# Kernel tuning notes

Measured on AMD Instinct MI355X. Metric: run time of the kernel, lower is better.

## Reference

```python
import jax, jax.numpy as jnp
import numpy as np
import itertools

SEQ, NF, K, SD, NB, NC, NOBJ = 8, 4, 3, 256, 512, 174, 10
BELTA, SUB, BATCH = 0.1, 10, 256
SCALES = list(range(NF, 0, -1))  # [4, 3, 2, 1]
D = (K + 1) * SD                 # per-frame fused feature dim = 1024


def _adjust_scales(seq_ind, is_test):
    # mirrors adjust_scale_train / adjust_scale_test
    scale_max = NF * 2
    if seq_ind < scale_max:
        return SCALES[-seq_ind:] if is_test else SCALES[-min(SUB, seq_ind):]
    return SCALES[:min(SUB, seq_ind) + 1]


def _plan(is_test):
    # Static (non-traced) relation-index plan: for each seq_ind, the set of
    # arithmetic-progression frame combinations selected by select_idx().
    plan = []
    for seq_ind in range(1, SEQ + 1):
        entries = []
        for scale in _adjust_scales(seq_ind, is_test):
            k = min(scale, seq_ind)
            division = seq_ind // scale
            sel = [r for r in itertools.combinations(range(seq_ind), k)
                   if np.all(np.diff(np.asarray(r)) == division)]
            if sel:
                entries.append((scale, np.asarray(sel, dtype=np.int32)))
        plan.append(entries)
    return plan


def _temporal_variation(init_input):
    # VLAD-style soft residuals. Source runs kmeans (non-deterministic,
    # numpy/detached); we use deterministic centers = first K points per clip
    # and reproduce the exact downstream math, including the (buggy but
    # faithful) scalar spectral-norm soft assignment shared by all points.
    x = init_input.reshape(-1, SEQ, NOBJ, SD)              # (B, S, O, d)
    flat = x.reshape(x.shape[0], SEQ * NOBJ, SD)           # (B, N, d)
    centers = flat[:, :K, :]                               # (B, K, d)
    diff = flat[:, None, :, :] - centers[:, :, None, :]    # (B, K, N, d)
    sig = jnp.linalg.svd(diff, compute_uv=False)[..., 0]   # matrix 2-norm per (b, k)
    w = jax.nn.softmax(-BELTA * sig ** 2, axis=-1)         # (B, K), same for every point
    # S[b,t,k,:] = sum_o w[b,k] * (x[b,t,o,:] - c[b,k,:])
    var = w[:, None, :, None] * (x.sum(axis=2)[:, :, None, :] - NOBJ * centers[:, None, :, :])
    return jax.lax.stop_gradient(var)  # source detaches via .detach().numpy()


def _fusion(x, w1, b1, w2, b2):
    # Sequential(ReLU, Linear, ReLU, Linear)
    h = jnp.maximum(jax.nn.relu(x) @ w1 + b1, 0.0)
    return h @ w2 + b2


def _forward(graph_out, init_input, params, is_test):
    B = graph_out.shape[0]
    var = _temporal_variation(init_input)                      # (B, S, K, d)
    new_input = jnp.concatenate([var.reshape(B, SEQ, K * SD), graph_out], axis=2)  # (B, S, D)
    rows = []
    for entries in _plan(bool(is_test)):
        acc = jnp.zeros((B, NC), graph_out.dtype)
        for scale, rel in entries:
            # batched gather of all sampled relations at once: (B, R, scale, D)
            g = new_input[:, rel, :].reshape(B, rel.shape[0], scale * D)
            acc = acc + _fusion(g, *params[scale]).sum(axis=1)
        rows.append(acc)
    return jnp.stack(rows, axis=1).reshape(B * SEQ, NC)


def setup_inputs():
    key = jax.random.key(0)
    ks = jax.random.split(key, 2 + 2 * len(SCALES))
    inp = {
        "graph_out": jax.random.normal(ks[0], (BATCH, SEQ, SD), jnp.float32),
        "init_input": jax.random.normal(ks[1], (BATCH * SEQ, NOBJ, SD), jnp.float32),
        "is_test": 0,
    }
    for i, s in enumerate(SCALES):
        inp[f"w1_{s}"] = jax.random.normal(ks[2 + 2 * i], (s * D, NB), jnp.float32) * 0.02
        inp[f"b1_{s}"] = jnp.zeros((NB,), jnp.float32)
        inp[f"w2_{s}"] = jax.random.normal(ks[3 + 2 * i], (NB, NC), jnp.float32) * 0.02
        inp[f"b2_{s}"] = jnp.zeros((NC,), jnp.float32)
    return inp


def reference(graph_out, init_input, is_test, w1_4, b1_4, w2_4, b2_4, w1_3, b1_3, w2_3, b2_3, w1_2, b1_2, w2_2, b2_2, w1_1, b1_1, w2_1, b2_1):
    params = {4: (w1_4, b1_4, w2_4, b2_4), 3: (w1_3, b1_3, w2_3, b2_3),
              2: (w1_2, b1_2, w2_2, b2_2), 1: (w1_1, b1_1, w2_1, b2_1)}
    return _forward(graph_out, init_input, params, is_test)
```

## Files before the change

### kernel.cpp

```cpp
#include <hip/hip_runtime.h>
#include <math.h>
#include <stdint.h>


typedef __attribute__((ext_vector_type(8))) short short8v;
typedef __attribute__((ext_vector_type(4))) short short4v;
typedef __attribute__((ext_vector_type(4))) float f32x4;

__device__ __forceinline__ short f2bf(float f) {
  uint32_t u = __float_as_uint(f);
  u += 0x7fffu + ((u >> 16) & 1u);
  return (short)(u >> 16);
}
__device__ __forceinline__ float bf2f(short s) {
  return __uint_as_float(((uint32_t)(uint16_t)s) << 16);
}
__device__ __forceinline__ void gload16(const void* g, void* l) {
  __builtin_amdgcn_global_load_lds(
      (const __attribute__((address_space(1))) void*)g,
      (__attribute__((address_space(3))) void*)l, 16, 0, 0);
}

__device__ const int8_t ROWS4[12][5] = {
  {3, 0,1,2,3},
  {4, 0,1,2,3},{4, 1,2,3,4},
  {5, 0,1,2,3},{5, 1,2,3,4},{5, 2,3,4,5},
  {6, 0,1,2,3},{6, 1,2,3,4},{6, 2,3,4,5},{6, 3,4,5,6},
  {7, 0,2,4,6},{7, 1,3,5,7},
};
__device__ const int8_t ROWS3[15][4] = {
  {2, 0,1,2},
  {3, 0,1,2},{3, 1,2,3},
  {4, 0,1,2},{4, 1,2,3},{4, 2,3,4},
  {5, 0,2,4},{5, 1,3,5},
  {6, 0,2,4},{6, 1,3,5},{6, 2,4,6},
  {7, 0,2,4},{7, 1,3,5},{7, 2,4,6},{7, 3,5,7},
};
__device__ const int8_t ROWS2[19][3] = {
  {1, 0,1},
  {2, 0,1},{2, 1,2},
  {3, 0,2},{3, 1,3},
  {4, 0,2},{4, 1,3},{4, 2,4},
  {5, 0,3},{5, 1,4},{5, 2,5},
  {6, 0,3},{6, 1,4},{6, 2,5},{6, 3,6},
  {7, 0,4},{7, 1,5},{7, 2,6},{7, 3,7},
};
__device__ const int8_t ROWS1[36][2] = {
  {0,0},
  {1,0},{1,1},
  {2,0},{2,1},{2,2},
  {3,0},{3,1},{3,2},{3,3},
  {4,0},{4,1},{4,2},{4,3},{4,4},
  {5,0},{5,1},{5,2},{5,3},{5,4},{5,5},
  {6,0},{6,1},{6,2},{6,3},{6,4},{6,5},{6,6},
  {7,0},{7,1},{7,2},{7,3},{7,4},{7,5},{7,6},{7,7},
};
__device__ const float CNT[8][4] = {
  {0,0,0,1},{0,0,1,2},{0,1,2,3},{1,2,2,4},
  {2,3,3,5},{3,2,3,6},{4,3,4,7},{2,4,4,8},
};

__device__ const int SL_LO[10]  = {0,1,2,3, 0,1,2, 0,1, 0};
__device__ const int SL_LEN[10] = {4,4,4,5, 4,5,6, 4,7, 8};
__device__ const int SL_PB[10]  = {0,4,8,12,17,21,26,32,36,43};
__device__ const int SL_MT[10]  = {0,8,16,24,34,42,52,64,72,86};

#define GV_FH    0
#define GV_FL    20480
#define GV_S     40960
#define GV_XSUM  67840
#define GV_VB    76032
#define GV_UU    78048
#define GV_SCAL  79008
#define GV_SZ    79056

__global__ __launch_bounds__(256) void gram_var(
    const float* __restrict__ init, const float* __restrict__ graph,
    short* __restrict__ Rbuf)
{
  __shared__ __align__(16) char smem[GV_SZ];
  short* Fh  = (short*)(smem + GV_FH);
  short* Fl  = (short*)(smem + GV_FL);
  float* Sm  = (float*)(smem + GV_S);
  float* xsm = (float*)(smem + GV_XSUM);
  float* vb  = (float*)(smem + GV_VB);
  float* uum = (float*)(smem + GV_UU);
  float* scal= (float*)(smem + GV_SCAL);

  const int tid = threadIdx.x, lane = tid & 63, w = tid >> 6;
  const int b = blockIdx.x;
  const float* fb = init + (size_t)b * 80 * 256;

  int ti_[7], tj_[7];
#pragma unroll
  for (int q = 0; q < 7; ++q) {
    int tt = w + q * 4;
    int t5 = (tt < 25) ? tt : 0;
    ti_[q] = t5 / 5; tj_[q] = t5 % 5;
  }

  f32x4 acc[7];
#pragma unroll
  for (int q = 0; q < 7; ++q) acc[q] = (f32x4){0.f, 0.f, 0.f, 0.f};

  for (int ch = 0; ch < 2; ++ch) {
    __syncthreads();
    {
      const int t = tid >> 5, kq = tid & 31;
      const float* src = fb + (size_t)(t * 10) * 256 + ch * 128 + kq * 4;
      f32x4 sum = (f32x4){0.f, 0.f, 0.f, 0.f};
#pragma unroll
      for (int o = 0; o < 10; ++o) {
        f32x4 v = *(const f32x4*)(src + (size_t)o * 256);
        int r = t * 10 + o;
        int byte8 = r * 256 + ((kq * 8) ^ ((r & 7) << 4));
        short4v hv, lv;
#pragma unroll
        for (int e = 0; e < 4; ++e) {
          short h = f2bf(v[e]);
          hv[e] = h;
          lv[e] = f2bf(v[e] - bf2f(h));
        }
        *(short4v*)((char*)Fh + byte8) = hv;
        *(short4v*)((char*)Fl + byte8) = lv;
        sum += v;
      }
      *(f32x4*)(xsm + t * 256 + ch * 128 + kq * 4) = sum;
    }
    __syncthreads();

#pragma unroll
    for (int ks = 0; ks < 4; ++ks) {
      const int koff2 = (ks * 32 + (lane >> 4) * 8) * 2;
#pragma unroll
      for (int q = 0; q < 7; ++q) {
        const int tt = w + q * 4;
        if (tt < 25) {
          int ra = ti_[q] * 16 + (lane & 15);
          int rb = tj_[q] * 16 + (lane & 15);
          int ba = ra * 256 + (koff2 ^ ((ra & 7) << 4));
          int bb = rb * 256 + (koff2 ^ ((rb & 7) << 4));
          short8v ah = *(const short8v*)((char*)Fh + ba);
          short8v al = *(const short8v*)((char*)Fl + ba);
          short8v bh = *(const short8v*)((char*)Fh + bb);
          short8v bl = *(const short8v*)((char*)Fl + bb);
          acc[q] = __builtin_amdgcn_mfma_f32_16x16x32_bf16(ah, bh, acc[q], 0, 0, 0);
          acc[q] = __builtin_amdgcn_mfma_f32_16x16x32_bf16(ah, bl, acc[q], 0, 0, 0);
          acc[q] = __builtin_amdgcn_mfma_f32_16x16x32_bf16(al, bh, acc[q], 0, 0, 0);
        }
      }
    }
  }

#pragma unroll
  for (int q = 0; q < 7; ++q) {
    const int tt = w + q * 4;
    if (tt < 25) {
      int row0 = ti_[q] * 16 + (lane >> 4) * 4;
      int col = tj_[q] * 16 + (lane & 15);
#pragma unroll
      for (int r = 0; r < 4; ++r) Sm[(row0 + r) * 84 + col] = acc[q][r];
    }
  }
  if (tid < 240) vb[(0 * 3 + tid / 80) * 84 + (tid % 80)] = 1.0f;
  __syncthreads();

  const int pk = (tid < 240) ? tid / 80 : 0;
  const int pi = (tid < 240) ? tid % 80 : 0;
  int cur = 0;
  for (int it = 0; it < 5; ++it) {
    const bool last = (it == 4);
    float u = 0.f;
    if (tid < 240) {
      const float* Si = Sm + pi * 84;
      const float* vk = vb + (cur * 3 + pk) * 84;
#pragma unroll
      for (int q2 = 0; q2 < 20; ++q2) {
        f32x4 aa = *(const f32x4*)(Si + q2 * 4);
        f32x4 vv = *(const f32x4*)(vk + q2 * 4);
        u += aa.x * vv.x + aa.y * vv.y + aa.z * vv.z + aa.w * vv.w;
      }
    } else if (tid < 246) {
      int w2 = tid - 240;
      int k = (w2 < 3) ? w2 : w2 - 3;
      const float* vk = vb + (cur * 3 + k) * 84;
      float s = 0.f;
      if (w2 < 3) {
        for (int j2 = 0; j2 < 80; ++j2) s += vk[j2];
        scal[k] = s;
      } else {
        const float* Sk = Sm + k * 84;
        for (int j2 = 0; j2 < 80; ++j2) s += Sk[j2] * vk[j2];
        scal[3 + k] = s;
      }
    }
    __syncthreads();
    if (tid < 240) {
      float sg = scal[pk], tu = scal[3 + pk];
      float un = u - Sm[pi * 84 + pk] * sg - tu + Sm[pk * 84 + pk] * sg;
      if (!last) vb[((cur ^ 1) * 3 + pk) * 84 + pi] = un * 6.103515625e-05f;
      else       uum[pk * 80 + pi] = un;
    }
    __syncthreads();
    if (!last) cur ^= 1;
  }

  if (tid < 192) {
    const int k = tid >> 6, ln = tid & 63;
    float v1 = vb[(cur * 3 + k) * 84 + ln];
    float u1 = uum[k * 80 + ln];
    float a = u1 * v1, b2 = v1 * v1;
    if (ln < 16) {
      float v2 = vb[(cur * 3 + k) * 84 + 64 + ln];
      float u2 = uum[k * 80 + 64 + ln];
      a += u2 * v2; b2 += v2 * v2;
    }
#pragma unroll
    for (int m = 32; m >= 1; m >>= 1) {
      a += __shfl_xor(a, m);
      b2 += __shfl_xor(b2, m);
    }
    if (ln == 0) scal[9 + k] = a / b2;
  }
  __syncthreads();
  if (tid == 0) {
    float L0 = -0.1f * scal[9], L1 = -0.1f * scal[10], L2 = -0.1f * scal[11];
    float m = fmaxf(L0, fmaxf(L1, L2));
    float e0 = expf(L0 - m), e1 = expf(L1 - m), e2 = expf(L2 - m);
    float inv = 1.0f / (e0 + e1 + e2);
    scal[6] = e0 * inv; scal[7] = e1 * inv; scal[8] = e2 * inv;
  }
  __syncthreads();

  {
    const float w0 = scal[6], w1 = scal[7], w2 = scal[8];
    const int d0 = (tid & 63) * 4;
#pragma unroll
    for (int p = 0; p < 2; ++p) {
      const int t = p * 4 + (tid >> 6);
      f32x4 xs = *(const f32x4*)(xsm + t * 256 + d0);
      f32x4 c0 = *(const f32x4*)(fb + 0 * 256 + d0);
      f32x4 c1 = *(const f32x4*)(fb + 1 * 256 + d0);
      f32x4 c2 = *(const f32x4*)(fb + 2 * 256 + d0);
      f32x4 go = *(const f32x4*)(graph + (size_t)(b * 8 + t) * 256 + d0);
      size_t rb = ((size_t)(b * 8 + t)) * 1024;
      short4v s0, s1, s2, s3;
#pragma unroll
      for (int q = 0; q < 4; ++q) {
        float xq = xs[q];
        s0[q] = f2bf(fmaxf(w0 * (xq - 10.f * c0[q]), 0.f));
        s1[q] = f2bf(fmaxf(w1 * (xq - 10.f * c1[q]), 0.f));
        s2[q] = f2bf(fmaxf(w2 * (xq - 10.f * c2[q]), 0.f));
        s3[q] = f2bf(fmaxf(go[q], 0.f));
      }
      *(short4v*)&Rbuf[rb + 0 + d0]   = s0;
      *(short4v*)&Rbuf[rb + 256 + d0] = s1;
      *(short4v*)&Rbuf[rb + 512 + d0] = s2;
      *(short4v*)&Rbuf[rb + 768 + d0] = s3;
    }
  }
}

__global__ __launch_bounds__(512) void prep_weights(
    const float* __restrict__ w1_4, const float* __restrict__ w1_3,
    const float* __restrict__ w1_2, const float* __restrict__ w1_1,
    const float* __restrict__ w2a, const float* __restrict__ w2b,
    const float* __restrict__ w2c, const float* __restrict__ w2d,
    short* __restrict__ W1T, short* __restrict__ W2T)
{
  __shared__ float sh[64 * 65];
  const int blk = blockIdx.x, tid = threadIdx.x;
  if (blk < 1280) {
    const int slice = blk >> 7, rem = blk & 127;
    const int k0 = (rem & 15) * 64, c0 = (rem >> 4) * 64;
    const float* W1; int j;
    if (slice < 4)      { W1 = w1_4; j = slice; }
    else if (slice < 7) { W1 = w1_3; j = slice - 4; }
    else if (slice < 9) { W1 = w1_2; j = slice - 7; }
    else                { W1 = w1_1; j = 0; }
#pragma unroll
    for (int q = tid; q < 1024; q += 512) {
      int r = q >> 4, cq = (q & 15) * 4;
      f32x4 v = *(const f32x4*)(W1 + (size_t)(j * 1024 + k0 + r) * 512 + c0 + cq);
      sh[r * 65 + cq + 0] = v.x; sh[r * 65 + cq + 1] = v.y;
      sh[r * 65 + cq + 2] = v.z; sh[r * 65 + cq + 3] = v.w;
    }
    __syncthreads();
#pragma unroll
    for (int q = tid; q < 1024; q += 512) {
      int cc = q >> 4, kq = (q & 15) * 4;
      short4v sv;
#pragma unroll
      for (int m = 0; m < 4; ++m) sv[m] = f2bf(sh[(kq + m) * 65 + cc]);
      *(short4v*)&W1T[(size_t)(slice * 512 + c0 + cc) * 1024 + k0 + kq] = sv;
    }
  } else {
    int idx = (blk - 1280) * 2048 + tid * 4;
    int col = idx >> 11, kg = idx & 2047;
    int si = kg >> 9, kr = kg & 511;
    const float* w = (si == 0) ? w2a : (si == 1) ? w2b : (si == 2) ? w2c : w2d;
    short4v sv;
#pragma unroll
    for (int q = 0; q < 4; ++q)
      sv[q] = (col < 174) ? f2bf(w[(size_t)(kr + q) * 174 + col]) : (short)0;
    *(short4v*)&W2T[idx] = sv;
  }
}

__global__ __launch_bounds__(256) void p_mfma(
    const short* __restrict__ A, const short* __restrict__ W1T,
    short* __restrict__ P)
{
  __shared__ short As[128 * 32];
  __shared__ short Bs[128 * 32];
  const int id = blockIdx.x;
  const int nid = (id & 7) * 51 + (id >> 3);
  const int ctile = nid & 3;
  const int rest = nid >> 2;
  int sl = 0;
#pragma unroll
  for (int q = 1; q < 10; ++q) if (rest >= SL_MT[q]) sl = q;
  const int mt = rest - SL_MT[sl];
  const int lo = SL_LO[sl];
  const unsigned len = (unsigned)SL_LEN[sl];
  short* Pp = P + (size_t)SL_PB[sl] * 131072;
  const short* Bp = W1T + ((size_t)sl * 512 + (size_t)ctile * 128) * 1024;

  const int tid = threadIdx.x, lane = tid & 63, w = tid >> 6;
  const int wr = w >> 1, wc = w & 1;
  const int rA = w * 16 + (lane >> 2);
  const int kkA = (lane & 3) * 8;
  const unsigned lr0 = (unsigned)(mt * 128 + rA), lr1 = lr0 + 64u;
  const int gr0 = (int)((lr0 / len) * 8u + lo + (lr0 % len));
  const int gr1 = (int)((lr1 / len) * 8u + lo + (lr1 % len));

  f32x4 acc[4][4];
#pragma unroll
  for (int m = 0; m < 4; ++m)
#pragma unroll
    for (int n = 0; n < 4; ++n) acc[m][n] = (f32x4){0.f, 0.f, 0.f, 0.f};

  for (int k0 = 0; k0 < 1024; k0 += 32) {
    __syncthreads();
    gload16(A + (size_t)gr0 * 1024 + k0 + kkA, As + w * 512);
    gload16(A + (size_t)gr1 * 1024 + k0 + kkA, As + 2048 + w * 512);
    gload16(Bp + (size_t)rA * 1024 + k0 + kkA, Bs + w * 512);
    gload16(Bp + (size_t)(64 + rA) * 1024 + k0 + kkA, Bs + 2048 + w * 512);
    __syncthreads();
    short8v a[4], bv[4];
#pragma unroll
    for (int m = 0; m < 4; ++m)
      a[m] = *(const short8v*)(As + (wr * 64 + m * 16 + (lane & 15)) * 32 + (lane >> 4) * 8);
#pragma unroll
    for (int n = 0; n < 4; ++n)
      bv[n] = *(const short8v*)(Bs + (wc * 64 + n * 16 + (lane & 15)) * 32 + (lane >> 4) * 8);
#pragma unroll
    for (int m = 0; m < 4; ++m)
#pragma unroll
      for (int n = 0; n < 4; ++n)
        acc[m][n] = __builtin_amdgcn_mfma_f32_16x16x32_bf16(a[m], bv[n], acc[m][n], 0, 0, 0);
  }

#pragma unroll
  for (int m = 0; m < 4; ++m) {
    int lrow = mt * 128 + wr * 64 + m * 16 + (lane >> 4) * 4;
#pragma unroll
    for (int n = 0; n < 4; ++n) {
      int col = ctile * 128 + wc * 64 + n * 16 + (lane & 15);
#pragma unroll
      for (int r = 0; r < 4; ++r)
        Pp[(size_t)(lrow + r) * 512 + col] = f2bf(acc[m][n][r]);
    }
  }
}

__global__ __launch_bounds__(256) void hsum_all(
    const short* __restrict__ P,
    const float* __restrict__ b1a, const float* __restrict__ b1b,
    const float* __restrict__ b1c, const float* __restrict__ b1d,
    short* __restrict__ Hsum)
{
  const int tid = threadIdx.x;
  const int row = blockIdx.x * 2 + (tid >> 7);
  const int t = row & 7;
  const size_t bq = (size_t)(row >> 3);
  const int c0 = (tid & 127) * 4;

  {
    const int pb[4] = {0, 4 * 131072, 8 * 131072, 12 * 131072};
    const int lo[4] = {0, 1, 2, 3};
    const int ln[4] = {4, 4, 4, 5};
    f32x4 bb = *(const f32x4*)(b1a + c0);
    f32x4 a = (f32x4){0.f, 0.f, 0.f, 0.f};
    for (int r = 0; r < 12; ++r) {
      if (ROWS4[r][0] != t) continue;
      f32x4 h = bb;
#pragma unroll
      for (int jj = 0; jj < 4; ++jj) {
        const short4v pv = *(const short4v*)(P + pb[jj] +
            (bq * ln[jj] + (ROWS4[r][1 + jj] - lo[jj])) * 512 + c0);
#pragma unroll
        for (int e = 0; e < 4; ++e) h[e] += bf2f(pv[e]);
      }
#pragma unroll
      for (int e = 0; e < 4; ++e) a[e] += fmaxf(h[e], 0.f);
    }
    short4v sv;
#pragma unroll
    for (int e = 0; e < 4; ++e) sv[e] = f2bf(a[e]);
    *(short4v*)&Hsum[(size_t)row * 2048 + c0] = sv;
  }
  {
    const int pb[3] = {17 * 131072, 21 * 131072, 26 * 131072};
    const int lo[3] = {0, 1, 2};
    const int ln[3] = {4, 5, 6};
    f32x4 bb = *(const f32x4*)(b1b + c0);
    f32x4 a = (f32x4){0.f, 0.f, 0.f, 0.f};
    for (int r = 0; r < 15; ++r) {
      if (ROWS3[r][0] != t) continue;
      f32x4 h = bb;
#pragma unroll
      for (int jj = 0; jj < 3; ++jj) {
        const short4v pv = *(const short4v*)(P + pb[jj] +
            (bq * ln[jj] + (ROWS3[r][1 + jj] - lo[jj])) * 512 + c0);
#pragma unroll
        for (int e = 0; e < 4; ++e) h[e] += bf2f(pv[e]);
      }
#pragma unroll
      for (int e = 0; e < 4; ++e) a[e] += fmaxf(h[e], 0.f);
    }
    short4v sv;
#pragma unroll
    for (int e = 0; e < 4; ++e) sv[e] = f2bf(a[e]);
    *(short4v*)&Hsum[(size_t)row * 2048 + 512 + c0] = sv;
  }
  {
    const int pb[2] = {32 * 131072, 36 * 131072};
    const int lo[2] = {0, 1};
    const int ln[2] = {4, 7};
    f32x4 bb = *(const f32x4*)(b1c + c0);
    f32x4 a = (f32x4){0.f, 0.f, 0.f, 0.f};
    for (int r = 0; r < 19; ++r) {
      if (ROWS2[r][0] != t) continue;
      f32x4 h = bb;
#pragma unroll
      for (int jj = 0; jj < 2; ++jj) {
        const short4v pv = *(const short4v*)(P + pb[jj] +
            (bq * ln[jj] + (ROWS2[r][1 + jj] - lo[jj])) * 512 + c0);
#pragma unroll
        for (int e = 0; e < 4; ++e) h[e] += bf2f(pv[e]);
      }
#pragma unroll
      for (int e = 0; e < 4; ++e) a[e] += fmaxf(h[e], 0.f);
    }
    short4v sv;
#pragma unroll
    for (int e = 0; e < 4; ++e) sv[e] = f2bf(a[e]);
    *(short4v*)&Hsum[(size_t)row * 2048 + 1024 + c0] = sv;
  }
  {
    f32x4 bb = *(const f32x4*)(b1d + c0);
    f32x4 a = (f32x4){0.f, 0.f, 0.f, 0.f};
    for (int r = 0; r < 36; ++r) {
      if (ROWS1[r][0] != t) continue;
      const short4v pv = *(const short4v*)(P + 43 * 131072 +
          (bq * 8 + ROWS1[r][1]) * 512 + c0);
#pragma unroll
      for (int e = 0; e < 4; ++e) a[e] += fmaxf(bb[e] + bf2f(pv[e]), 0.f);
    }
    short4v sv;
#pragma unroll
    for (int e = 0; e < 4; ++e) sv[e] = f2bf(a[e]);
    *(short4v*)&Hsum[(size_t)row * 2048 + 1536 + c0] = sv;
  }
}

__global__ __launch_bounds__(256) void out_split(
    const short* __restrict__ H, const short* __restrict__ W2T,
    float* __restrict__ partial)
{
  __shared__ short As[128 * 32];
  __shared__ short Bs[64 * 32];
  const int tid = threadIdx.x, lane = tid & 63, w = tid >> 6;
  const int wr = w >> 1, wc = w & 1;
  const int rowBase = blockIdx.y * 128, colBase = blockIdx.x * 64;
  const int kBase = blockIdx.z * 512;
  const int rA = w * 16 + (lane >> 2);
  const int kkA = (lane & 3) * 8;

  f32x4 acc[4][2];
#pragma unroll
  for (int m = 0; m < 4; ++m)
#pragma unroll
    for (int n = 0; n < 2; ++n) acc[m][n] = (f32x4){0.f, 0.f, 0.f, 0.f};

  for (int k0 = 0; k0 < 512; k0 += 32) {
    const int kg = kBase + k0;
    __syncthreads();
    gload16(H + (size_t)(rowBase + rA) * 2048 + kg + kkA, As + w * 512);
    gload16(H + (size_t)(rowBase + 64 + rA) * 2048 + kg + kkA, As + 2048 + w * 512);
    gload16(W2T + (size_t)(colBase + rA) * 2048 + kg + kkA, Bs + w * 512);
    __syncthreads();
    short8v a[4], bv[2];
#pragma unroll
    for (int m = 0; m < 4; ++m)
      a[m] = *(const short8v*)(As + (wr * 64 + m * 16 + (lane & 15)) * 32 + (lane >> 4) * 8);
#pragma unroll
    for (int n = 0; n < 2; ++n)
      bv[n] = *(const short8v*)(Bs + (wc * 32 + n * 16 + (lane & 15)) * 32 + (lane >> 4) * 8);
#pragma unroll
    for (int m = 0; m < 4; ++m)
#pragma unroll
      for (int n = 0; n < 2; ++n)
        acc[m][n] = __builtin_amdgcn_mfma_f32_16x16x32_bf16(a[m], bv[n], acc[m][n], 0, 0, 0);
  }

  float* pz = partial + (size_t)blockIdx.z * 2048 * 192;
#pragma unroll
  for (int n = 0; n < 2; ++n) {
    int col = colBase + wc * 32 + n * 16 + (lane & 15);
#pragma unroll
    for (int m = 0; m < 4; ++m) {
      int row0 = rowBase + wr * 64 + m * 16 + (lane >> 4) * 4;
#pragma unroll
      for (int r = 0; r < 4; ++r)
        pz[(size_t)(row0 + r) * 192 + col] = acc[m][n][r];
    }
  }
}

__global__ __launch_bounds__(256) void out_reduce(
    const float* __restrict__ partial,
    const float* __restrict__ b2a, const float* __restrict__ b2b,
    const float* __restrict__ b2c, const float* __restrict__ b2d,
    float* __restrict__ out)
{
  const int row = blockIdx.x, col = threadIdx.x;
  if (col >= 174) return;
  const size_t o = (size_t)row * 192 + col;
  float s = partial[o] + partial[o + (size_t)2048 * 192]
          + partial[o + (size_t)4096 * 192] + partial[o + (size_t)6144 * 192];
  int tt = row & 7;
  float bias = CNT[tt][0] * b2a[col] + CNT[tt][1] * b2b[col]
             + CNT[tt][2] * b2c[col] + CNT[tt][3] * b2d[col];
  out[(size_t)row * 174 + col] = s + bias;
}

extern "C" void kernel_launch(void* const* d_in, const int* in_sizes, int n_in,
                              void* d_out, int out_size, void* d_ws, size_t ws_size,
                              hipStream_t stream) {
  const float* graph = (const float*)d_in[0];
  const float* init  = (const float*)d_in[1];
  const float* w1[4] = {(const float*)d_in[3],  (const float*)d_in[7],
                        (const float*)d_in[11], (const float*)d_in[15]};
  const float* b1[4] = {(const float*)d_in[4],  (const float*)d_in[8],
                        (const float*)d_in[12], (const float*)d_in[16]};
  const float* w2[4] = {(const float*)d_in[5],  (const float*)d_in[9],
                        (const float*)d_in[13], (const float*)d_in[17]};
  const float* b2[4] = {(const float*)d_in[6],  (const float*)d_in[10],
                        (const float*)d_in[14], (const float*)d_in[18]};
  float* out = (float*)d_out;

  char* ws = (char*)d_ws;
  short* Rbf  = (short*)(ws + 0);
  short* W1T  = (short*)(ws + ((size_t)4  << 20));
  short* P    = (short*)(ws + ((size_t)14 << 20));
  short* W2T  = (short*)(ws + ((size_t)34 << 20));
  short* Hsum = (short*)(ws + 0);
  float* Part = (float*)(ws + ((size_t)8 << 20));

  gram_var<<<256, 256, 0, stream>>>(init, graph, Rbf);

  prep_weights<<<1472, 512, 0, stream>>>(w1[0], w1[1], w1[2], w1[3],
                                         w2[0], w2[1], w2[2], w2[3], W1T, W2T);

  p_mfma<<<408, 256, 0, stream>>>(Rbf, W1T, P);

  hsum_all<<<1024, 256, 0, stream>>>(P, b1[0], b1[1], b1[2], b1[3], Hsum);

  out_split<<<dim3(3, 16, 4), 256, 0, stream>>>(Hsum, W2T, Part);

  out_reduce<<<2048, 256, 0, stream>>>(Part, b2[0], b2[1], b2[2], b2[3], out);
}
```

Baseline: 98.14 us.

## Stage full features in LDS once and run power iteration per-wavefront without block barriers

The feature tile is now converted to split bf16 hi/lo and written to LDS in one pass covering all 256 columns, removing the two-chunk load/compute loop and its extra barriers. The Gram MFMA loop then runs over the whole K dimension at once. The power iteration for the three cluster-center spectral norms is restructured so that each of three wavefronts owns one center and keeps its vector in registers. Reductions use shuffles, which removes the block-wide __syncthreads per iteration. LDS usage grows to about 118 KB per block, which may limit occupancy, and the Gram row stride changes to 86.

New measurement: 101.3 us. +3.2%, slower.

```diff
diff --git a/kernel.cpp b/kernel.cpp
--- a/kernel.cpp
+++ b/kernel.cpp
@@ -66,13 +66,12 @@
 __device__ const int SL_MT[10]  = {0,8,16,24,34,42,52,64,72,86};
 
 #define GV_FH    0
-#define GV_FL    20480
-#define GV_S     40960
-#define GV_XSUM  67840
-#define GV_VB    76032
-#define GV_UU    78048
-#define GV_SCAL  79008
-#define GV_SZ    79056
+#define GV_FL    40960
+#define GV_S     81920
+#define GV_XSUM  109440
+#define GV_VK    117632
+#define GV_SCAL  118656
+#define GV_SZ    118704
 
 __global__ __launch_bounds__(256) void gram_var(
     const float* __restrict__ init, const float* __restrict__ graph,
@@ -83,13 +82,40 @@
   short* Fl  = (short*)(smem + GV_FL);
   float* Sm  = (float*)(smem + GV_S);
   float* xsm = (float*)(smem + GV_XSUM);
-  float* vb  = (float*)(smem + GV_VB);
-  float* uum = (float*)(smem + GV_UU);
+  float* vkb = (float*)(smem + GV_VK);
   float* scal= (float*)(smem + GV_SCAL);
 
   const int tid = threadIdx.x, lane = tid & 63, w = tid >> 6;
   const int b = blockIdx.x;
   const float* fb = init + (size_t)b * 80 * 256;
+
+  {
+    const int t = tid >> 5, kq0 = tid & 31;
+#pragma unroll
+    for (int h = 0; h < 2; ++h) {
+      const int cq = kq0 + h * 32;
+      const float* src = fb + (size_t)(t * 10) * 256 + cq * 4;
+      f32x4 sum = (f32x4){0.f, 0.f, 0.f, 0.f};
+#pragma unroll
+      for (int o = 0; o < 10; ++o) {
+        f32x4 v = *(const f32x4*)(src + (size_t)o * 256);
+        int r = t * 10 + o;
+        int byte8 = r * 512 + ((cq * 8) ^ ((r & 7) << 4));
+        short4v hv, lv;
+#pragma unroll
+        for (int e = 0; e < 4; ++e) {
+          short hx = f2bf(v[e]);
+          hv[e] = hx;
+          lv[e] = f2bf(v[e] - bf2f(hx));
+        }
+        *(short4v*)((char*)Fh + byte8) = hv;
+        *(short4v*)((char*)Fl + byte8) = lv;
+        sum += v;
+      }
+      *(f32x4*)(xsm + t * 256 + cq * 4) = sum;
+    }
+  }
+  __syncthreads();
 
   int ti_[7], tj_[7];
 #pragma unroll
@@ -98,60 +124,31 @@
     int t5 = (tt < 25) ? tt : 0;
     ti_[q] = t5 / 5; tj_[q] = t5 % 5;
   }
-
   f32x4 acc[7];
 #pragma unroll
   for (int q = 0; q < 7; ++q) acc[q] = (f32x4){0.f, 0.f, 0.f, 0.f};
 
-  for (int ch = 0; ch < 2; ++ch) {
-    __syncthreads();
-    {
-      const int t = tid >> 5, kq = tid & 31;
-      const float* src = fb + (size_t)(t * 10) * 256 + ch * 128 + kq * 4;
-      f32x4 sum = (f32x4){0.f, 0.f, 0.f, 0.f};
-#pragma unroll
-      for (int o = 0; o < 10; ++o) {
-        f32x4 v = *(const f32x4*)(src + (size_t)o * 256);
-        int r = t * 10 + o;
-        int byte8 = r * 256 + ((kq * 8) ^ ((r & 7) << 4));
-        short4v hv, lv;
-#pragma unroll
-        for (int e = 0; e < 4; ++e) {
-          short h = f2bf(v[e]);
-          hv[e] = h;
-          lv[e] = f2bf(v[e] - bf2f(h));
-        }
-        *(short4v*)((char*)Fh + byte8) = hv;
-        *(short4v*)((char*)Fl + byte8) = lv;
-        sum += v;
-      }
-      *(f32x4*)(xsm + t * 256 + ch * 128 + kq * 4) = sum;
-    }
-    __syncthreads();
-
-#pragma unroll
-    for (int ks = 0; ks < 4; ++ks) {
-      const int koff2 = (ks * 32 + (lane >> 4) * 8) * 2;
-#pragma unroll
-      for (int q = 0; q < 7; ++q) {
-        const int tt = w + q * 4;
-        if (tt < 25) {
-          int ra = ti_[q] * 16 + (lane & 15);
-          int rb = tj_[q] * 16 + (lane & 15);
-          int ba = ra * 256 + (koff2 ^ ((ra & 7) << 4));
-          int bb = rb * 256 + (koff2 ^ ((rb & 7) << 4));
-          short8v ah = *(const short8v*)((char*)Fh + ba);
-          short8v al = *(const short8v*)((char*)Fl + ba);
-          short8v bh = *(const short8v*)((char*)Fh + bb);
-          short8v bl = *(const short8v*)((char*)Fl + bb);
-          acc[q] = __builtin_amdgcn_mfma_f32_16x16x32_bf16(ah, bh, acc[q], 0, 0, 0);
-          acc[q] = __builtin_amdgcn_mfma_f32_16x16x32_bf16(ah, bl, acc[q], 0, 0, 0);
-          acc[q] = __builtin_amdgcn_mfma_f32_16x16x32_bf16(al, bh, acc[q], 0, 0, 0);
-        }
-      }
-    }
-  }
-
+#pragma unroll
+  for (int ks = 0; ks < 8; ++ks) {
+    const int koff = ks * 64 + (lane >> 4) * 16;
+#pragma unroll
+    for (int q = 0; q < 7; ++q) {
+      const int tt = w + q * 4;
+      if (tt < 25) {
+        int ra = ti_[q] * 16 + (lane & 15);
+        int rb = tj_[q] * 16 + (lane & 15);
+        int ba = ra * 512 + (koff ^ ((ra & 7) << 4));
+        int bb = rb * 512 + (koff ^ ((rb & 7) << 4));
+        short8v ah = *(const short8v*)((char*)Fh + ba);
+        short8v al = *(const short8v*)((char*)Fl + ba);
+        short8v bh = *(const short8v*)((char*)Fh + bb);
+        short8v bl = *(const short8v*)((char*)Fl + bb);
+        acc[q] = __builtin_amdgcn_mfma_f32_16x16x32_bf16(ah, bh, acc[q], 0, 0, 0);
+        acc[q] = __builtin_amdgcn_mfma_f32_16x16x32_bf16(ah, bl, acc[q], 0, 0, 0);
+        acc[q] = __builtin_amdgcn_mfma_f32_16x16x32_bf16(al, bh, acc[q], 0, 0, 0);
+      }
+    }
+  }
 #pragma unroll
   for (int q = 0; q < 7; ++q) {
     const int tt = w + q * 4;
@@ -159,68 +156,67 @@
       int row0 = ti_[q] * 16 + (lane >> 4) * 4;
       int col = tj_[q] * 16 + (lane & 15);
 #pragma unroll
-      for (int r = 0; r < 4; ++r) Sm[(row0 + r) * 84 + col] = acc[q][r];
-    }
-  }
-  if (tid < 240) vb[(0 * 3 + tid / 80) * 84 + (tid % 80)] = 1.0f;
+      for (int r = 0; r < 4; ++r) Sm[(row0 + r) * 86 + col] = acc[q][r];
+    }
+  }
   __syncthreads();
 
-  const int pk = (tid < 240) ? tid / 80 : 0;
-  const int pi = (tid < 240) ? tid % 80 : 0;
-  int cur = 0;
-  for (int it = 0; it < 5; ++it) {
-    const bool last = (it == 4);
-    float u = 0.f;
-    if (tid < 240) {
-      const float* Si = Sm + pi * 84;
-      const float* vk = vb + (cur * 3 + pk) * 84;
-#pragma unroll
-      for (int q2 = 0; q2 < 20; ++q2) {
-        f32x4 aa = *(const f32x4*)(Si + q2 * 4);
-        f32x4 vv = *(const f32x4*)(vk + q2 * 4);
-        u += aa.x * vv.x + aa.y * vv.y + aa.z * vv.z + aa.w * vv.w;
-      }
-    } else if (tid < 246) {
-      int w2 = tid - 240;
-      int k = (w2 < 3) ? w2 : w2 - 3;
-      const float* vk = vb + (cur * 3 + k) * 84;
-      float s = 0.f;
-      if (w2 < 3) {
-        for (int j2 = 0; j2 < 80; ++j2) s += vk[j2];
-        scal[k] = s;
+  if (w < 3) {
+    const int k = w;
+    float* vk = vkb + k * 84;
+    const bool has2 = (lane < 16);
+    const int r0 = lane, r1 = 64 + lane;
+    const float S0k = Sm[r0 * 86 + k];
+    const float S1k = has2 ? Sm[r1 * 86 + k] : 0.f;
+    const float Skl = Sm[k * 86 + r0];
+    const float Skh = has2 ? Sm[k * 86 + r1] : 0.f;
+    const float Skk = Sm[k * 86 + k];
+    const float* Sr0 = Sm + r0 * 86;
+    const float* Sr1 = Sm + r1 * 86;
+
+    float v0 = 1.f, v1 = 1.f;
+    vk[r0] = 1.f;
+    if (has2) vk[r1] = 1.f;
+
+    float u0f = 0.f, u1f = 0.f;
+    for (int it = 0; it < 5; ++it) {
+      float u0 = 0.f, u1 = 0.f;
+#pragma unroll
+      for (int q = 0; q < 40; ++q) {
+        float2 vv = *(const float2*)(vk + q * 2);
+        float2 a0 = *(const float2*)(Sr0 + q * 2);
+        u0 += a0.x * vv.x + a0.y * vv.y;
+        if (has2) {
+          float2 a1 = *(const float2*)(Sr1 + q * 2);
+          u1 += a1.x * vv.x + a1.y * vv.y;
+        }
+      }
+      float sg = v0 + (has2 ? v1 : 0.f);
+      float tu = Skl * v0 + (has2 ? Skh * v1 : 0.f);
+#pragma unroll
+      for (int m = 32; m >= 1; m >>= 1) {
+        sg += __shfl_xor(sg, m);
+        tu += __shfl_xor(tu, m);
+      }
+      float un0 = u0 - S0k * sg - tu + Skk * sg;
+      float un1 = u1 - S1k * sg - tu + Skk * sg;
+      if (it < 4) {
+        v0 = un0 * 6.103515625e-05f;
+        v1 = un1 * 6.103515625e-05f;
+        vk[r0] = v0;
+        if (has2) vk[r1] = v1;
       } else {
-        const float* Sk = Sm + k * 84;
-        for (int j2 = 0; j2 < 80; ++j2) s += Sk[j2] * vk[j2];
-        scal[3 + k] = s;
-      }
-    }
-    __syncthreads();
-    if (tid < 240) {
-      float sg = scal[pk], tu = scal[3 + pk];
-      float un = u - Sm[pi * 84 + pk] * sg - tu + Sm[pk * 84 + pk] * sg;
-      if (!last) vb[((cur ^ 1) * 3 + pk) * 84 + pi] = un * 6.103515625e-05f;
-      else       uum[pk * 80 + pi] = un;
-    }
-    __syncthreads();
-    if (!last) cur ^= 1;
-  }
-
-  if (tid < 192) {
-    const int k = tid >> 6, ln = tid & 63;
-    float v1 = vb[(cur * 3 + k) * 84 + ln];
-    float u1 = uum[k * 80 + ln];
-    float a = u1 * v1, b2 = v1 * v1;
-    if (ln < 16) {
-      float v2 = vb[(cur * 3 + k) * 84 + 64 + ln];
-      float u2 = uum[k * 80 + 64 + ln];
-      a += u2 * v2; b2 += v2 * v2;
-    }
+        u0f = un0; u1f = un1;
+      }
+    }
+    float a = u0f * v0 + (has2 ? u1f * v1 : 0.f);
+    float bq = v0 * v0 + (has2 ? v1 * v1 : 0.f);
 #pragma unroll
     for (int m = 32; m >= 1; m >>= 1) {
       a += __shfl_xor(a, m);
-      b2 += __shfl_xor(b2, m);
-    }
-    if (ln == 0) scal[9 + k] = a / b2;
+      bq += __shfl_xor(bq, m);
+    }
+    if (lane == 0) scal[9 + k] = a / bq;
   }
   __syncthreads();
   if (tid == 0) {
```
